# Kernel optimization log

Hardware: AMD Instinct MI355X
Metric: run time of the kernel (lower is better)

The kernel has to match this reference:

```python
import math
import jax, jax.numpy as jnp
import numpy as np

B, T, D, H = 4, 2048, 256, 4
DK = D // H
P = 2 * T - 1  # relative position length


def setup_inputs() -> dict:
    key = jax.random.key(0)
    ks = jax.random.split(key, 16)
    s = 0.02
    inp = {
        "query": jax.random.normal(ks[0], (B, T, D), jnp.float32),
        "key": jax.random.normal(ks[1], (B, T, D), jnp.float32),
        "value": jax.random.normal(ks[2], (B, T, D), jnp.float32),
        "pos_emb": jax.random.normal(ks[3], (1, P, D), jnp.float32),
        "mask": jnp.ones((B, 1, T), jnp.int32),
        "Wq": jax.random.normal(ks[4], (D, D), jnp.float32) * s,
        "bq": jnp.zeros((D,), jnp.float32),
        "Wk": jax.random.normal(ks[5], (D, D), jnp.float32) * s,
        "bk": jnp.zeros((D,), jnp.float32),
        "Wv": jax.random.normal(ks[6], (D, D), jnp.float32) * s,
        "bv": jnp.zeros((D,), jnp.float32),
        "Wpos": jax.random.normal(ks[7], (D, D), jnp.float32) * s,
        "pos_bias_u": jax.random.normal(ks[8], (H, DK), jnp.float32) * s,
        "pos_bias_v": jax.random.normal(ks[9], (H, DK), jnp.float32) * s,
        "Wo": jax.random.normal(ks[10], (D, D), jnp.float32) * s,
        "bo": jnp.zeros((D,), jnp.float32),
    }
    return inp


def rel_shift(x):
    # x: (B, H, T, P) with P = 2T-1  ->  (B, H, T, T)
    b, h, t, p = x.shape
    x_pad = jnp.pad(x, ((0, 0), (0, 0), (0, 0), (1, 0)))  # (B,H,T,P+1)
    x_pad = x_pad.reshape(b, h, p + 1, t)
    x = x_pad[:, :, 1:].reshape(b, h, t, p)
    return x[..., : p // 2 + 1]


def reference(query, key, value, pos_emb, mask, Wq, bq, Wk, bk, Wv, bv,
              Wpos, pos_bias_u, pos_bias_v, Wo, bo):
    b = query.shape[0]
    q = (query @ Wq.T + bq).reshape(b, -1, H, DK)              # (B,T,H,DK)
    k = (key @ Wk.T + bk).reshape(b, -1, H, DK).transpose(0, 2, 1, 3)    # (B,H,T,DK)
    v = (value @ Wv.T + bv).reshape(b, -1, H, DK).transpose(0, 2, 1, 3)  # (B,H,T,DK)
    p = (pos_emb @ Wpos.T).reshape(pos_emb.shape[0], -1, H, DK).transpose(0, 2, 1, 3)  # (1,H,P,DK)

    q_u = (q + pos_bias_u).transpose(0, 2, 1, 3)  # (B,H,T,DK)
    q_v = (q + pos_bias_v).transpose(0, 2, 1, 3)

    matrix_ac = jnp.matmul(q_u, k.transpose(0, 1, 3, 2))  # (B,H,T,T)
    matrix_bd = jnp.matmul(q_v, p.transpose(0, 1, 3, 2))  # (B,H,T,P), batch broadcast
    matrix_bd = rel_shift(matrix_bd)                       # (B,H,T,T)

    scores = (matrix_ac + matrix_bd) / math.sqrt(DK)
    m = (mask[:, None] == 0)  # (B,1,1,T) bool
    scores = jnp.where(m, jnp.float32(-1e9), scores)
    attn = jax.nn.softmax(scores, axis=-1)
    attn = jnp.where(m, jnp.float32(0.0), attn)

    x = jnp.matmul(attn, v)                               # (B,H,T,DK)
    x = x.transpose(0, 2, 1, 3).reshape(b, -1, H * DK)    # (B,T,D)
    return x @ Wo.T + bo
```

## Files before the change

### kernel.cpp

```cpp
#include <hip/hip_runtime.h>
#include <hip/hip_bf16.h>
#include <string.h>

#define Bc 4
#define Tc 2048
#define Dc 256
#define Hc 4
#define DKc 64
#define Pc 4095

typedef short bf16x8 __attribute__((ext_vector_type(8)));
typedef float f32x4 __attribute__((ext_vector_type(4)));

__device__ __forceinline__ unsigned short f2bs(float x) {
    __bf16 b = (__bf16)x;
    return __builtin_bit_cast(unsigned short, b);
}
__device__ __forceinline__ float bs2f(unsigned short u) {
    unsigned int x = ((unsigned int)u) << 16;
    return __builtin_bit_cast(float, x);
}

__device__ __forceinline__ void gemm_body(
    const float* __restrict__ A, const float* __restrict__ Wt,
    const float* __restrict__ bias, const float* __restrict__ addv,
    unsigned short* __restrict__ outp, int M, int Tdim, float scale,
    unsigned short* sa, unsigned short* sb)
{
    const int tid = threadIdx.x;
    const int wv = tid >> 6, lane = tid & 63;
    const int c = lane & 15, g = lane >> 4;
    const int m0 = blockIdx.x * 64, n0 = blockIdx.y * 64;
    const int tb = wv * 16;

    f32x4 acc[4];
    #pragma unroll
    for (int ct = 0; ct < 4; ct++) acc[ct] = (f32x4){0.f, 0.f, 0.f, 0.f};

    for (int k0 = 0; k0 < 256; k0 += 64) {
        if (k0) __syncthreads();
        #pragma unroll
        for (int r = 0; r < 2; r++) {
            int lin = tid + 256 * r;
            int row = lin >> 3, ch = lin & 7;
            int gm = m0 + row;
            float4 f0, f1;
            if (gm < M) {
                f0 = *(const float4*)(A + (size_t)gm * 256 + k0 + ch * 8);
                f1 = *(const float4*)(A + (size_t)gm * 256 + k0 + ch * 8 + 4);
            } else {
                f0 = make_float4(0.f, 0.f, 0.f, 0.f); f1 = f0;
            }
            unsigned short pa[8] = {f2bs(f0.x), f2bs(f0.y), f2bs(f0.z), f2bs(f0.w),
                                    f2bs(f1.x), f2bs(f1.y), f2bs(f1.z), f2bs(f1.w)};
            *(uint4*)&sa[row * 72 + ch * 8] = *(const uint4*)pa;

            float4 w0 = *(const float4*)(Wt + (size_t)(n0 + row) * 256 + k0 + ch * 8);
            float4 w1 = *(const float4*)(Wt + (size_t)(n0 + row) * 256 + k0 + ch * 8 + 4);
            unsigned short pb[8] = {f2bs(w0.x), f2bs(w0.y), f2bs(w0.z), f2bs(w0.w),
                                    f2bs(w1.x), f2bs(w1.y), f2bs(w1.z), f2bs(w1.w)};
            *(uint4*)&sb[row * 72 + ch * 8] = *(const uint4*)pb;
        }
        __syncthreads();
        #pragma unroll
        for (int kk = 0; kk < 2; kk++) {
            bf16x8 af = *(const bf16x8*)&sa[(tb + c) * 72 + kk * 32 + g * 8];
            #pragma unroll
            for (int ct = 0; ct < 4; ct++) {
                bf16x8 bf = *(const bf16x8*)&sb[(ct * 16 + c) * 72 + kk * 32 + g * 8];
                acc[ct] = __builtin_amdgcn_mfma_f32_16x16x32_bf16(af, bf, acc[ct], 0, 0, 0);
            }
        }
    }

    __syncthreads();
    #pragma unroll
    for (int ct = 0; ct < 4; ct++) {
        int n = n0 + ct * 16 + c;
        float badd = (bias ? bias[n] : 0.f) + (addv ? addv[n] : 0.f);
        #pragma unroll
        for (int r = 0; r < 4; r++)
            sa[(tb + g * 4 + r) * 72 + ct * 16 + c] = f2bs((acc[ct][r] + badd) * scale);
    }
    __syncthreads();
    const int hh = n0 >> 6;
    #pragma unroll
    for (int r = 0; r < 2; r++) {
        int lin = tid + 256 * r;
        int row = lin >> 3, ch = lin & 7;
        int gm = m0 + row;
        if (gm >= M) continue;
        int bb = gm / Tdim, t = gm - bb * Tdim;
        size_t oidx = ((size_t)(bb * Hc + hh) * Tdim + t) * DKc + ch * 8;
        *(uint4*)&outp[oidx] = *(const uint4*)&sa[row * 72 + ch * 8];
    }
}

__global__ __launch_bounds__(256) void gemm_qkv(
    const float* __restrict__ q, const float* __restrict__ k, const float* __restrict__ v,
    const float* __restrict__ Wq, const float* __restrict__ bq,
    const float* __restrict__ Wk, const float* __restrict__ bk,
    const float* __restrict__ Wv, const float* __restrict__ bv,
    const float* __restrict__ pbu,
    unsigned short* __restrict__ qo, unsigned short* __restrict__ ko,
    unsigned short* __restrict__ vo)
{
    __shared__ unsigned short sa[64 * 72];
    __shared__ unsigned short sb[64 * 72];
    const float *A, *Wt, *bias, *addv; unsigned short* outp; float scale;
    if (blockIdx.z == 0)      { A = q; Wt = Wq; bias = bq; addv = pbu;    outp = qo; scale = 0.125f; }
    else if (blockIdx.z == 1) { A = k; Wt = Wk; bias = bk; addv = nullptr; outp = ko; scale = 1.f; }
    else                      { A = v; Wt = Wv; bias = bv; addv = nullptr; outp = vo; scale = 1.f; }
    gemm_body(A, Wt, bias, addv, outp, Bc * Tc, Tc, scale, sa, sb);
}

__global__ __launch_bounds__(256) void gemm_p(
    const float* __restrict__ pos_emb, const float* __restrict__ Wpos,
    const float* __restrict__ pbu, const float* __restrict__ pbv,
    unsigned short* __restrict__ ph_b, float* __restrict__ dpw)
{
    __shared__ unsigned short sa[64 * 72];
    __shared__ unsigned short sb[64 * 72];
    gemm_body(pos_emb, Wpos, nullptr, nullptr, ph_b, Pc, Pc, 1.f, sa, sb);
    const int tid = threadIdx.x;
    const int m0 = blockIdx.x * 64, h = blockIdx.y;
    if (tid < 64) {
        int w = m0 + tid;
        if (w < Pc) {
            float acc = 0.f;
            #pragma unroll
            for (int dk = 0; dk < DKc; dk++)
                acc = fmaf(pbv[h * DKc + dk] - pbu[h * DKc + dk],
                           bs2f(sa[tid * 72 + dk]), acc);
            dpw[h * Pc + w] = acc * 0.125f;
        }
    }
}

__global__ __launch_bounds__(256) void gemm_out_split(
    const unsigned short* __restrict__ Ahi,
    const unsigned short* __restrict__ Alo,
    const float* __restrict__ Wo,
    const float* __restrict__ bias,
    float* __restrict__ outp, int M)
{
    __shared__ unsigned short sah[64 * 72];
    __shared__ unsigned short sal[64 * 72];
    __shared__ unsigned short sbh[64 * 72];
    __shared__ unsigned short sbl[64 * 72];
    __shared__ float sout[64 * 68];
    const int tid = threadIdx.x;
    const int wv = tid >> 6, lane = tid & 63;
    const int c = lane & 15, g = lane >> 4;
    const int m0 = blockIdx.x * 64, n0 = blockIdx.y * 64;
    const int tb = wv * 16;

    f32x4 acc[4];
    #pragma unroll
    for (int ct = 0; ct < 4; ct++) acc[ct] = (f32x4){0.f, 0.f, 0.f, 0.f};

    for (int k0 = 0; k0 < 256; k0 += 64) {
        if (k0) __syncthreads();
        #pragma unroll
        for (int r = 0; r < 2; r++) {
            int lin = tid + 256 * r;
            int row = lin >> 3, ch = lin & 7;
            size_t asrc = (size_t)(m0 + row) * 256 + k0 + ch * 8;
            *(uint4*)&sah[row * 72 + ch * 8] = *(const uint4*)(Ahi + asrc);
            *(uint4*)&sal[row * 72 + ch * 8] = *(const uint4*)(Alo + asrc);
            float4 w0 = *(const float4*)(Wo + (size_t)(n0 + row) * 256 + k0 + ch * 8);
            float4 w1 = *(const float4*)(Wo + (size_t)(n0 + row) * 256 + k0 + ch * 8 + 4);
            float we[8] = {w0.x, w0.y, w0.z, w0.w, w1.x, w1.y, w1.z, w1.w};
            unsigned short phi[8], plo[8];
            #pragma unroll
            for (int e = 0; e < 8; e++) {
                unsigned short hi = f2bs(we[e]);
                phi[e] = hi;
                plo[e] = f2bs(we[e] - bs2f(hi));
            }
            *(uint4*)&sbh[row * 72 + ch * 8] = *(const uint4*)phi;
            *(uint4*)&sbl[row * 72 + ch * 8] = *(const uint4*)plo;
        }
        __syncthreads();
        #pragma unroll
        for (int kk = 0; kk < 2; kk++) {
            bf16x8 ah = *(const bf16x8*)&sah[(tb + c) * 72 + kk * 32 + g * 8];
            bf16x8 al = *(const bf16x8*)&sal[(tb + c) * 72 + kk * 32 + g * 8];
            #pragma unroll
            for (int ct = 0; ct < 4; ct++) {
                bf16x8 bh = *(const bf16x8*)&sbh[(ct * 16 + c) * 72 + kk * 32 + g * 8];
                bf16x8 bl = *(const bf16x8*)&sbl[(ct * 16 + c) * 72 + kk * 32 + g * 8];
                acc[ct] = __builtin_amdgcn_mfma_f32_16x16x32_bf16(ah, bh, acc[ct], 0, 0, 0);
                acc[ct] = __builtin_amdgcn_mfma_f32_16x16x32_bf16(ah, bl, acc[ct], 0, 0, 0);
                acc[ct] = __builtin_amdgcn_mfma_f32_16x16x32_bf16(al, bh, acc[ct], 0, 0, 0);
            }
        }
    }

    __syncthreads();
    #pragma unroll
    for (int ct = 0; ct < 4; ct++) {
        float b = bias[n0 + ct * 16 + c];
        #pragma unroll
        for (int r = 0; r < 4; r++)
            sout[(tb + g * 4 + r) * 68 + ct * 16 + c] = acc[ct][r] + b;
    }
    __syncthreads();
    #pragma unroll
    for (int r = 0; r < 4; r++) {
        int lin = tid + 256 * r;
        int row = lin >> 4, c4 = lin & 15;
        float4 v = *(const float4*)&sout[row * 68 + c4 * 4];
        *(float4*)&outp[(size_t)(m0 + row) * 256 + n0 + c4 * 4] = v;
    }
}

__global__ __launch_bounds__(256) void attn_mfma(
    const unsigned short* __restrict__ qu,
    const unsigned short* __restrict__ kh,
    const unsigned short* __restrict__ vh,
    const unsigned short* __restrict__ ph,
    const float* __restrict__ dpw_g,
    const int*   __restrict__ mask,
    unsigned short* __restrict__ xhi,
    unsigned short* __restrict__ xlo)
{
    __shared__ unsigned short sq[64 * 72];
    __shared__ unsigned short sk[64 * 72];
    __shared__ unsigned short svt[64 * 72];
    __shared__ unsigned short sp[64 * 72];
    __shared__ unsigned short spw[128 * 72];
    __shared__ float sbdw[4][16 * 84];
    __shared__ float sdpw[128];
    __shared__ float smask[64];

    const int tid = threadIdx.x;
    const int wv = tid >> 6;
    const int lane = tid & 63;
    const int c = lane & 15, g = lane >> 4;
    const int bh = blockIdx.x, b = bh >> 2, h = bh & 3;
    const int t0 = blockIdx.y * 64;
    const int tb = wv * 16;
    const int base0 = Tc - 64 - t0;

    const unsigned short* qbase = qu + ((size_t)bh * Tc + t0) * DKc;
    const unsigned short* kbase = kh + (size_t)bh * Tc * DKc;
    const unsigned short* vbase = vh + (size_t)bh * Tc * DKc;
    const unsigned short* pbase = ph + (size_t)h * Pc * DKc;

    const int srow = tid >> 3, sch = tid & 7;

    #pragma unroll
    for (int r = 0; r < 2; r++) {
        int row = srow + r * 32;
        *(uint4*)&sq[row * 72 + sch * 8] =
            *(const uint4*)(qbase + (size_t)row * DKc + sch * 8);
        int a0 = base0 + row;
        *(uint4*)&spw[(a0 & 127) * 72 + sch * 8] =
            *(const uint4*)(pbase + (size_t)a0 * DKc + sch * 8);
    }
    if (tid < 64) sdpw[(base0 + tid) & 127] = dpw_g[h * Pc + base0 + tid];

    uint4 kreg[2], vreg[2], preg[2];
    float dpwreg = 0.f; int mreg = 1;
    #pragma unroll
    for (int r = 0; r < 2; r++) {
        int row = srow + r * 32;
        kreg[r] = *(const uint4*)(kbase + (size_t)row * DKc + sch * 8);
        vreg[r] = *(const uint4*)(vbase + (size_t)row * DKc + sch * 8);
        preg[r] = *(const uint4*)(pbase + (size_t)(base0 + 64 + row) * DKc + sch * 8);
    }
    if (tid < 64) {
        dpwreg = dpw_g[h * Pc + base0 + 64 + tid];
        mreg = mask[b * Tc + tid];
    }

    f32x4 O[4];
    #pragma unroll
    for (int ct = 0; ct < 4; ct++) O[ct] = (f32x4){0.f, 0.f, 0.f, 0.f};
    float mrow[4], lrow[4];
    #pragma unroll
    for (int r = 0; r < 4; r++) { mrow[r] = -3.0e38f; lrow[r] = 0.f; }

    bf16x8 qf0, qf1;

    for (int kt = 0; kt < Tc / 64; kt++) {
        const int relb = base0 + kt * 64;
        __syncthreads();

        #pragma unroll
        for (int r = 0; r < 2; r++) {
            int row = srow + r * 32;
            *(uint4*)&sk[row * 72 + sch * 8] = kreg[r];
            unsigned short el[8];
            __builtin_memcpy(el, &vreg[r], 16);
            #pragma unroll
            for (int e = 0; e < 8; e++) {
                int dk = sch * 8 + e;
                svt[dk * 72 + (row ^ ((dk >> 3) << 3))] = el[e];
            }
            *(uint4*)&spw[((relb + 64 + row) & 127) * 72 + sch * 8] = preg[r];
        }
        if (tid < 64) {
            sdpw[(relb + 64 + tid) & 127] = dpwreg;
            smask[tid] = (mreg == 0) ? -1e9f : 0.f;
        }
        __syncthreads();

        if (kt < Tc / 64 - 1) {
            const int j0n = (kt + 1) * 64;
            const int relbn = relb + 64;
            #pragma unroll
            for (int r = 0; r < 2; r++) {
                int row = srow + r * 32;
                kreg[r] = *(const uint4*)(kbase + (size_t)(j0n + row) * DKc + sch * 8);
                vreg[r] = *(const uint4*)(vbase + (size_t)(j0n + row) * DKc + sch * 8);
                preg[r] = *(const uint4*)(pbase + (size_t)(relbn + 64 + row) * DKc + sch * 8);
            }
            if (tid < 64) {
                dpwreg = dpw_g[h * Pc + relbn + 64 + tid];
                mreg = mask[b * Tc + j0n + tid];
            }
        }

        if (kt == 0) {
            qf0 = *(const bf16x8*)&sq[(tb + c) * 72 + g * 8];
            qf1 = *(const bf16x8*)&sq[(tb + c) * 72 + (4 + g) * 8];
        }

        f32x4 sac[4];
        #pragma unroll
        for (int ct = 0; ct < 4; ct++) {
            f32x4 acc = (f32x4){0.f, 0.f, 0.f, 0.f};
            bf16x8 kf0 = *(const bf16x8*)&sk[(ct * 16 + c) * 72 + g * 8];
            bf16x8 kf1 = *(const bf16x8*)&sk[(ct * 16 + c) * 72 + (4 + g) * 8];
            acc = __builtin_amdgcn_mfma_f32_16x16x32_bf16(qf0, kf0, acc, 0, 0, 0);
            acc = __builtin_amdgcn_mfma_f32_16x16x32_bf16(qf1, kf1, acc, 0, 0, 0);
            sac[ct] = acc;
        }

        #pragma unroll
        for (int wt = 0; wt < 5; wt++) {
            f32x4 acc = (f32x4){0.f, 0.f, 0.f, 0.f};
            int wlog = (48 - tb) + wt * 16 + c;
            int phys = (relb + wlog) & 127;
            bf16x8 pf0 = *(const bf16x8*)&spw[phys * 72 + g * 8];
            bf16x8 pf1 = *(const bf16x8*)&spw[phys * 72 + (4 + g) * 8];
            acc = __builtin_amdgcn_mfma_f32_16x16x32_bf16(qf0, pf0, acc, 0, 0, 0);
            acc = __builtin_amdgcn_mfma_f32_16x16x32_bf16(qf1, pf1, acc, 0, 0, 0);
            float dpwv = sdpw[phys];
            #pragma unroll
            for (int r = 0; r < 4; r++)
                sbdw[wv][(g * 4 + r) * 84 + wt * 16 + c] = acc[r] + dpwv;
        }

        float sreg[4][4];
        #pragma unroll
        for (int ct = 0; ct < 4; ct++) {
            float madd = smask[ct * 16 + c];
            #pragma unroll
            for (int r = 0; r < 4; r++) {
                int tt = g * 4 + r;
                int x = ct * 16 + c - tt + 15;
                sreg[ct][r] = sac[ct][r] + sbdw[wv][tt * 84 + x] + madd;
            }
        }

        float tmax[4], tsum[4];
        #pragma unroll
        for (int r = 0; r < 4; r++)
            tmax[r] = fmaxf(fmaxf(sreg[0][r], sreg[1][r]), fmaxf(sreg[2][r], sreg[3][r]));
        #pragma unroll
        for (int off = 1; off < 16; off <<= 1)
            #pragma unroll
            for (int r = 0; r < 4; r++)
                tmax[r] = fmaxf(tmax[r], __shfl_xor(tmax[r], off));

        float mnew[4], scl[4];
        #pragma unroll
        for (int r = 0; r < 4; r++) {
            mnew[r] = fmaxf(mrow[r], tmax[r]);
            scl[r] = __expf(mrow[r] - mnew[r]);
        }
        float pr[4][4];
        #pragma unroll
        for (int r = 0; r < 4; r++) {
            #pragma unroll
            for (int ct = 0; ct < 4; ct++)
                pr[ct][r] = __expf(sreg[ct][r] - mnew[r]);
            tsum[r] = (pr[0][r] + pr[1][r]) + (pr[2][r] + pr[3][r]);
        }
        #pragma unroll
        for (int off = 1; off < 16; off <<= 1)
            #pragma unroll
            for (int r = 0; r < 4; r++)
                tsum[r] += __shfl_xor(tsum[r], off);
        #pragma unroll
        for (int r = 0; r < 4; r++) {
            lrow[r] = lrow[r] * scl[r] + tsum[r];
            mrow[r] = mnew[r];
        }
        #pragma unroll
        for (int ct = 0; ct < 4; ct++) {
            f32x4 o = O[ct];
            o[0] *= scl[0]; o[1] *= scl[1]; o[2] *= scl[2]; o[3] *= scl[3];
            O[ct] = o;
        }

        #pragma unroll
        for (int ct = 0; ct < 4; ct++)
            #pragma unroll
            for (int r = 0; r < 4; r++)
                sp[(tb + g * 4 + r) * 72 + ct * 16 + c] = f2bs(pr[ct][r]);

        #pragma unroll
        for (int js = 0; js < 2; js++) {
            bf16x8 pfrag = *(const bf16x8*)&sp[(tb + c) * 72 + (js * 4 + g) * 8];
            #pragma unroll
            for (int ct = 0; ct < 4; ct++) {
                int dk = ct * 16 + c;
                int tcol = (js * 32 + g * 8) ^ ((dk >> 3) << 3);
                bf16x8 vf = *(const bf16x8*)&svt[dk * 72 + tcol];
                O[ct] = __builtin_amdgcn_mfma_f32_16x16x32_bf16(pfrag, vf, O[ct], 0, 0, 0);
            }
        }
    }

    float invl[4];
    #pragma unroll
    for (int r = 0; r < 4; r++)
        invl[r] = (lrow[r] > 0.f) ? 1.f / lrow[r] : 0.f;
    #pragma unroll
    for (int ct = 0; ct < 4; ct++)
        #pragma unroll
        for (int r = 0; r < 4; r++) {
            size_t idx = ((size_t)(b * Tc + t0 + tb + g * 4 + r)) * Dc + h * DKc + ct * 16 + c;
            float v = O[ct][r] * invl[r];
            unsigned short hi = f2bs(v);
            xhi[idx] = hi;
            xlo[idx] = f2bs(v - bs2f(hi));
        }
}

extern "C" void kernel_launch(void* const* d_in, const int* in_sizes, int n_in,
                              void* d_out, int out_size, void* d_ws, size_t ws_size,
                              hipStream_t stream) {
    const float* query   = (const float*)d_in[0];
    const float* key_    = (const float*)d_in[1];
    const float* value   = (const float*)d_in[2];
    const float* pos_emb = (const float*)d_in[3];
    const int*   mask    = (const int*)d_in[4];
    const float* Wq  = (const float*)d_in[5];
    const float* bq  = (const float*)d_in[6];
    const float* Wk  = (const float*)d_in[7];
    const float* bk  = (const float*)d_in[8];
    const float* Wv  = (const float*)d_in[9];
    const float* bv  = (const float*)d_in[10];
    const float* Wpos = (const float*)d_in[11];
    const float* pbu = (const float*)d_in[12];
    const float* pbv = (const float*)d_in[13];
    const float* Wo  = (const float*)d_in[14];
    const float* bo  = (const float*)d_in[15];
    float* out = (float*)d_out;

    const size_t NQ = (size_t)Bc * Hc * Tc * DKc;
    unsigned short* qu_b = (unsigned short*)d_ws;
    unsigned short* kh_b = qu_b + NQ;
    unsigned short* vh_b = kh_b + NQ;
    unsigned short* ph_b = vh_b + NQ;
    unsigned short* xhi  = ph_b + 1048576;
    unsigned short* xlo  = xhi + NQ;
    float* dpw = (float*)(xlo + NQ);

    dim3 blk(256);
    gemm_qkv<<<dim3(128, 4, 3), blk, 0, stream>>>(query, key_, value,
        Wq, bq, Wk, bk, Wv, bv, pbu, qu_b, kh_b, vh_b);
    gemm_p<<<dim3(64, 4), blk, 0, stream>>>(pos_emb, Wpos, pbu, pbv, ph_b, dpw);
    attn_mfma<<<dim3(Bc * Hc, Tc / 64), blk, 0, stream>>>(qu_b, kh_b, vh_b, ph_b, dpw, mask, xhi, xlo);
    gemm_out_split<<<dim3(128, 4), blk, 0, stream>>>(xhi, xlo, Wo, bo, out, Bc * Tc);
}
```

Baseline: 245.8 us.

## Enlarge attention query tile to 128 rows with 8 waves, drop register prefetch

The attention kernel now processes 128 query rows per block with 512 threads (8 waves), so each K/V/P tile loaded into shared memory is reused by twice as many waves. The register-based prefetch of the next K/V/P tile is removed in favour of direct loads each iteration. Wave priority is raised around the MFMA sections. The larger tile halves the grid (256 blocks) and raises shared memory per block, which may reduce occupancy, and losing the prefetch exposes global load latency.

```diff
diff --git a/kernel.cpp b/kernel.cpp
--- a/kernel.cpp
+++ b/kernel.cpp
@@ -215,7 +215,7 @@
     }
 }
 
-__global__ __launch_bounds__(256) void attn_mfma(
+__global__ __launch_bounds__(512) void attn_mfma(
     const unsigned short* __restrict__ qu,
     const unsigned short* __restrict__ kh,
     const unsigned short* __restrict__ vh,
@@ -225,13 +225,13 @@
     unsigned short* __restrict__ xhi,
     unsigned short* __restrict__ xlo)
 {
-    __shared__ unsigned short sq[64 * 72];
+    __shared__ unsigned short sq[128 * 72];
     __shared__ unsigned short sk[64 * 72];
     __shared__ unsigned short svt[64 * 72];
-    __shared__ unsigned short sp[64 * 72];
-    __shared__ unsigned short spw[128 * 72];
-    __shared__ float sbdw[4][16 * 84];
-    __shared__ float sdpw[128];
+    __shared__ unsigned short sp[128 * 72];
+    __shared__ unsigned short spw[256 * 72];
+    __shared__ float sbdw[8][16 * 84];
+    __shared__ float sdpw[256];
     __shared__ float smask[64];
 
     const int tid = threadIdx.x;
@@ -239,9 +239,9 @@
     const int lane = tid & 63;
     const int c = lane & 15, g = lane >> 4;
     const int bh = blockIdx.x, b = bh >> 2, h = bh & 3;
-    const int t0 = blockIdx.y * 64;
+    const int t0 = blockIdx.y * 128;
     const int tb = wv * 16;
-    const int base0 = Tc - 64 - t0;
+    const int base0 = Tc - 128 - t0;
 
     const unsigned short* qbase = qu + ((size_t)bh * Tc + t0) * DKc;
     const unsigned short* kbase = kh + (size_t)bh * Tc * DKc;
@@ -252,28 +252,15 @@
 
     #pragma unroll
     for (int r = 0; r < 2; r++) {
-        int row = srow + r * 32;
-        *(uint4*)&sq[row * 72 + sch * 8] =
-            *(const uint4*)(qbase + (size_t)row * DKc + sch * 8);
+        int lin = tid + 512 * r;
+        int row = lin >> 3, ch = lin & 7;
+        *(uint4*)&sq[row * 72 + ch * 8] =
+            *(const uint4*)(qbase + (size_t)row * DKc + ch * 8);
         int a0 = base0 + row;
-        *(uint4*)&spw[(a0 & 127) * 72 + sch * 8] =
-            *(const uint4*)(pbase + (size_t)a0 * DKc + sch * 8);
-    }
-    if (tid < 64) sdpw[(base0 + tid) & 127] = dpw_g[h * Pc + base0 + tid];
-
-    uint4 kreg[2], vreg[2], preg[2];
-    float dpwreg = 0.f; int mreg = 1;
-    #pragma unroll
-    for (int r = 0; r < 2; r++) {
-        int row = srow + r * 32;
-        kreg[r] = *(const uint4*)(kbase + (size_t)row * DKc + sch * 8);
-        vreg[r] = *(const uint4*)(vbase + (size_t)row * DKc + sch * 8);
-        preg[r] = *(const uint4*)(pbase + (size_t)(base0 + 64 + row) * DKc + sch * 8);
-    }
-    if (tid < 64) {
-        dpwreg = dpw_g[h * Pc + base0 + 64 + tid];
-        mreg = mask[b * Tc + tid];
-    }
+        *(uint4*)&spw[(a0 & 255) * 72 + ch * 8] =
+            *(const uint4*)(pbase + (size_t)a0 * DKc + ch * 8);
+    }
+    if (tid < 128) sdpw[(base0 + tid) & 255] = dpw_g[h * Pc + base0 + tid];
 
     f32x4 O[4];
     #pragma unroll
@@ -285,49 +272,41 @@
     bf16x8 qf0, qf1;
 
     for (int kt = 0; kt < Tc / 64; kt++) {
+        const int j0 = kt * 64;
         const int relb = base0 + kt * 64;
         __syncthreads();
 
-        #pragma unroll
-        for (int r = 0; r < 2; r++) {
-            int row = srow + r * 32;
-            *(uint4*)&sk[row * 72 + sch * 8] = kreg[r];
+        *(uint4*)&sk[srow * 72 + sch * 8] =
+            *(const uint4*)(kbase + (size_t)(j0 + srow) * DKc + sch * 8);
+        {
+            uint4 raw = *(const uint4*)(vbase + (size_t)(j0 + srow) * DKc + sch * 8);
             unsigned short el[8];
-            __builtin_memcpy(el, &vreg[r], 16);
+            __builtin_memcpy(el, &raw, 16);
             #pragma unroll
             for (int e = 0; e < 8; e++) {
                 int dk = sch * 8 + e;
-                svt[dk * 72 + (row ^ ((dk >> 3) << 3))] = el[e];
-            }
-            *(uint4*)&spw[((relb + 64 + row) & 127) * 72 + sch * 8] = preg[r];
+                svt[dk * 72 + (srow ^ ((dk >> 3) << 3))] = el[e];
+            }
+        }
+        {
+            int pabs = relb + 128 + srow;
+            int psrc = pabs <= Pc - 1 ? pabs : Pc - 1;
+            *(uint4*)&spw[(pabs & 255) * 72 + sch * 8] =
+                *(const uint4*)(pbase + (size_t)psrc * DKc + sch * 8);
         }
         if (tid < 64) {
-            sdpw[(relb + 64 + tid) & 127] = dpwreg;
-            smask[tid] = (mreg == 0) ? -1e9f : 0.f;
+            int da = relb + 128 + tid;
+            sdpw[da & 255] = dpw_g[h * Pc + (da <= Pc - 1 ? da : Pc - 1)];
+            smask[tid] = (mask[b * Tc + j0 + tid] == 0) ? -1e9f : 0.f;
         }
         __syncthreads();
-
-        if (kt < Tc / 64 - 1) {
-            const int j0n = (kt + 1) * 64;
-            const int relbn = relb + 64;
-            #pragma unroll
-            for (int r = 0; r < 2; r++) {
-                int row = srow + r * 32;
-                kreg[r] = *(const uint4*)(kbase + (size_t)(j0n + row) * DKc + sch * 8);
-                vreg[r] = *(const uint4*)(vbase + (size_t)(j0n + row) * DKc + sch * 8);
-                preg[r] = *(const uint4*)(pbase + (size_t)(relbn + 64 + row) * DKc + sch * 8);
-            }
-            if (tid < 64) {
-                dpwreg = dpw_g[h * Pc + relbn + 64 + tid];
-                mreg = mask[b * Tc + j0n + tid];
-            }
-        }
 
         if (kt == 0) {
             qf0 = *(const bf16x8*)&sq[(tb + c) * 72 + g * 8];
             qf1 = *(const bf16x8*)&sq[(tb + c) * 72 + (4 + g) * 8];
         }
 
+        __builtin_amdgcn_s_setprio(1);
         f32x4 sac[4];
         #pragma unroll
         for (int ct = 0; ct < 4; ct++) {
@@ -339,11 +318,12 @@
             sac[ct] = acc;
         }
 
+        const int wstart = 112 - tb;
         #pragma unroll
         for (int wt = 0; wt < 5; wt++) {
             f32x4 acc = (f32x4){0.f, 0.f, 0.f, 0.f};
-            int wlog = (48 - tb) + wt * 16 + c;
-            int phys = (relb + wlog) & 127;
+            int plog = wstart + wt * 16 + c;
+            int phys = (relb + plog) & 255;
             bf16x8 pf0 = *(const bf16x8*)&spw[phys * 72 + g * 8];
             bf16x8 pf1 = *(const bf16x8*)&spw[phys * 72 + (4 + g) * 8];
             acc = __builtin_amdgcn_mfma_f32_16x16x32_bf16(qf0, pf0, acc, 0, 0, 0);
@@ -353,6 +333,7 @@
             for (int r = 0; r < 4; r++)
                 sbdw[wv][(g * 4 + r) * 84 + wt * 16 + c] = acc[r] + dpwv;
         }
+        __builtin_amdgcn_s_setprio(0);
 
         float sreg[4][4];
         #pragma unroll
@@ -413,6 +394,7 @@
             for (int r = 0; r < 4; r++)
                 sp[(tb + g * 4 + r) * 72 + ct * 16 + c] = f2bs(pr[ct][r]);
 
+        __builtin_amdgcn_s_setprio(1);
         #pragma unroll
         for (int js = 0; js < 2; js++) {
             bf16x8 pfrag = *(const bf16x8*)&sp[(tb + c) * 72 + (js * 4 + g) * 8];
@@ -424,6 +406,7 @@
                 O[ct] = __builtin_amdgcn_mfma_f32_16x16x32_bf16(pfrag, vf, O[ct], 0, 0, 0);
             }
         }
+        __builtin_amdgcn_s_setprio(0);
     }
 
     float invl[4];
@@ -472,10 +455,10 @@
     unsigned short* xlo  = xhi + NQ;
     float* dpw = (float*)(xlo + NQ);
 
-    dim3 blk(256);
-    gemm_qkv<<<dim3(128, 4, 3), blk, 0, stream>>>(query, key_, value,
+    gemm_qkv<<<dim3(128, 4, 3), dim3(256), 0, stream>>>(query, key_, value,
         Wq, bq, Wk, bk, Wv, bv, pbu, qu_b, kh_b, vh_b);
-    gemm_p<<<dim3(64, 4), blk, 0, stream>>>(pos_emb, Wpos, pbu, pbv, ph_b, dpw);
-    attn_mfma<<<dim3(Bc * Hc, Tc / 64), blk, 0, stream>>>(qu_b, kh_b, vh_b, ph_b, dpw, mask, xhi, xlo);
-    gemm_out_split<<<dim3(128, 4), blk, 0, stream>>>(xhi, xlo, Wo, bo, out, Bc * Tc);
-}
+    gemm_p<<<dim3(64, 4), dim3(256), 0, stream>>>(pos_emb, Wpos, pbu, pbv, ph_b, dpw);
+    attn_mfma<<<dim3(Bc * Hc, Tc / 128), dim3(512), 0, stream>>>(
+        qu_b, kh_b, vh_b, ph_b, dpw, mask, xhi, xlo);
+    gemm_out_split<<<dim3(128, 4), dim3(256), 0, stream>>>(xhi, xlo, Wo, bo, out, Bc * Tc);
+}
```

Result: faster. 223.8 us (-8.9%).
